# Performance work log

Hardware: AMD Instinct MI355X
Metric: run time of the kernel (lower is better)

Reference implementation:

```python
import jax, jax.numpy as jnp
import numpy as np

B, S = 64, 256
F, H, V = 512, 2048, 32000
PAD = 0
LN_EPS = 1e-5


def setup_inputs() -> dict:
    key = jax.random.key(0)
    ks = jax.random.split(key, 10)
    inputs = jax.random.randint(ks[0], (B, S), 0, V, dtype=jnp.int64)
    targets = jax.random.randint(ks[1], (B, S), 0, V, dtype=jnp.int64)
    # parameters (kaiming-ish / torch-default-ish scales)
    see = jax.random.normal(ks[2], (2 * F, F), jnp.float32) * (2.0 / (2 * F)) ** 0.5
    bias = jnp.zeros((F,), jnp.float32)
    W_in = jax.random.normal(ks[3], (H, F), jnp.float32) * (1.0 / F) ** 0.5
    b_in = jnp.zeros((H,), jnp.float32)
    W_out = jax.random.normal(ks[4], (F, H), jnp.float32) * (1.0 / H) ** 0.5
    b_out = jnp.zeros((F,), jnp.float32)
    ln_g = jnp.ones((F,), jnp.float32)
    ln_b = jnp.zeros((F,), jnp.float32)
    emb = jax.random.normal(ks[5], (V, F), jnp.float32)
    return {"inputs": inputs, "targets": targets, "see": see, "bias": bias,
            "W_in": W_in, "b_in": b_in, "W_out": W_out, "b_out": b_out,
            "ln_g": ln_g, "ln_b": ln_b, "emb": emb}


def _layernorm(x, g, b):
    mu = jnp.mean(x, axis=-1, keepdims=True)
    var = jnp.mean((x - mu) ** 2, axis=-1, keepdims=True)
    return (x - mu) * jax.lax.rsqrt(var + LN_EPS) * g + b


def reference(inputs, targets, see, bias, W_in, b_in, W_out, b_out, ln_g, ln_b, emb):
    emb_m = emb.at[PAD].set(0.0)  # padding_idx row is zero
    inv_sqrt_f = 1.0 / (F ** 0.5)

    def step(state, xy):
        idx, tgt = xy                      # [B], [B]
        vecs = emb_m[idx]                  # [B,F]
        gate = jax.nn.sigmoid(jnp.concatenate([vecs, state], axis=-1) @ see + bias)
        cont = state * gate + vecs * (1.0 - gate)
        h = jax.nn.relu(_layernorm(cont, ln_g, ln_b) @ W_in.T + b_in)
        out = h @ W_out.T + b_out          # [B,F]
        logits = (out @ emb_m.T) * inv_sqrt_f  # [B,V]
        logp = jax.nn.log_softmax(logits, axis=-1)
        nll = -jnp.take_along_axis(logp, tgt[:, None], axis=1)[:, 0]
        mask = (tgt != PAD).astype(logits.dtype)
        li = jnp.sum(nll * mask) / jnp.maximum(jnp.sum(mask), 1.0)
        return cont, li

    xs = (inputs.T, targets.T)  # [S,B]
    _, losses = jax.lax.scan(step, jnp.zeros((inputs.shape[0], F), emb.dtype), xs)
    return jnp.mean(losses)
```

## Files before the change

kernel.cpp:

```cpp
#include <hip/hip_runtime.h>
#include <hip/hip_fp8.h>

#define F_DIM 512
#define H_DIM 2048
#define V_DIM 32000
#define B_DIM 64
#define S_DIM 256
#define ROWS (S_DIM*B_DIM)
#define NT_LOG 250
#define SCALE 0.04419417382415922f
#define LSE_OFF 40.0f

typedef __attribute__((ext_vector_type(8))) short  short8;
typedef __attribute__((ext_vector_type(4))) float  floatx4;
typedef __attribute__((ext_vector_type(4))) int    intx4;
typedef __attribute__((ext_vector_type(8))) int    i32x8;
typedef __attribute__((ext_vector_type(4))) unsigned int uix4;

static __device__ inline unsigned short f2bf(float x){
  unsigned int u = __float_as_uint(x);
  u += 0x7fffu + ((u >> 16) & 1u);
  return (unsigned short)(u >> 16);
}
static __device__ inline float bf2f(unsigned short u){
  return __uint_as_float(((unsigned int)u) << 16);
}
static __device__ inline unsigned char f2fp8(float x){
  __hip_fp8_e4m3 q(x);
  return q.__x;
}
static __device__ inline int sw8(int row, int col){
  int g = (col >> 3) & 7;
  int chunk = ((g >> 1) ^ ((row >> 1) & 3));
  int lob = (g & 1) ^ ((row >> 3) & 1);
  return (col & ~63) | (chunk << 4) | (lob << 3) | (col & 7);
}
static __device__ inline int zvperm(int c){
  return (c & ~63) | ((c & 15) << 2) | ((c >> 4) & 3);
}
static __device__ inline float wsum(float v){
  #pragma unroll
  for(int m = 32; m > 0; m >>= 1) v += __shfl_xor(v, m);
  return v;
}
static __device__ inline void load_lds16(const void* g, void* l){
  __builtin_amdgcn_global_load_lds((const __attribute__((address_space(1))) void*)g,
                                   (__attribute__((address_space(3))) void*)l, 16, 0, 0);
}

__global__ __launch_bounds__(256) void cast_w(const float* __restrict__ src,
                                              unsigned short* __restrict__ dst, int n){
  int i = blockIdx.x*256 + threadIdx.x;
  int stride = gridDim.x*256;
  for(; i < n; i += stride) dst[i] = f2bf(src[i]);
}
__global__ __launch_bounds__(256) void cast_emb(const float* __restrict__ src,
    unsigned short* __restrict__ dst, unsigned char* __restrict__ d8){
  int i = blockIdx.x*256 + threadIdx.x;
  int stride = gridDim.x*256;
  for(; i < V_DIM*F_DIM; i += stride){
    float v = (i < F_DIM) ? 0.f : src[i];
    dst[i] = f2bf(v);
    int row = i >> 9, col = i & 511;
    d8[(long)row*512 + sw8(row, col)] = f2fp8(v);
  }
}

__global__ __launch_bounds__(256) void prep_see(const float* __restrict__ see,
    unsigned short* __restrict__ TT, unsigned char* __restrict__ B8){
  int n = blockIdx.x;
  for(int k = threadIdx.x; k < 512; k += 256){
    TT[n*512 + k] = f2bf(see[(long)k*512 + n]);
    B8[n*512 + k] = f2fp8(see[(long)(512+k)*512 + n]);
  }
}

__global__ __launch_bounds__(256) void gather_vecs(const float* __restrict__ emb,
    const int* __restrict__ inp, unsigned short* __restrict__ V){
  long row = (long)blockIdx.x*4 + (threadIdx.x >> 6);
  int l = threadIdx.x & 63;
  int t = (int)(row >> 6), b = (int)(row & 63);
  int idx = inp[b*S_DIM + t];
  short8 o;
  if (idx == 0){
    #pragma unroll
    for(int i=0;i<8;i++) o[i] = 0;
  } else {
    const float* e = emb + (long)idx*F_DIM + l*8;
    float4 a = *(const float4*)e;
    float4 bq = *(const float4*)(e + 4);
    o[0]=(short)f2bf(a.x); o[1]=(short)f2bf(a.y); o[2]=(short)f2bf(a.z); o[3]=(short)f2bf(a.w);
    o[4]=(short)f2bf(bq.x);o[5]=(short)f2bf(bq.y);o[6]=(short)f2bf(bq.z);o[7]=(short)f2bf(bq.w);
  }
  *(short8*)(V + row*F_DIM + l*8) = o;
}

__global__ __launch_bounds__(512, 1) void recurrence_batch(
    const unsigned int* __restrict__ ZV,
    const unsigned char* __restrict__ W8,
    unsigned short* __restrict__ CONTB)
{
  __shared__ unsigned char stt[2][16][560];

  const int tid = threadIdx.x;
  const int w  = tid >> 6;
  const int l  = tid & 63;
  const int rl = l & 15, rq = l >> 4;
  const int wg = blockIdx.x;
  const int colb = w*64;

  i32x8 Bfr[4][4];
  #pragma unroll
  for(int kt=0;kt<4;kt++)
    #pragma unroll
    for(int tl=0;tl<4;tl++)
      Bfr[kt][tl] = *(const i32x8*)(W8 + (long)(colb + tl*16 + rl)*512 + kt*128 + rq*32);

  float s_old[16];
  #pragma unroll
  for(int i=0;i<16;i++) s_old[i] = 0.f;

  const unsigned int* zbase = ZV + (long)(wg*16 + rq*4)*512 + colb + rl*4;
  unsigned short* cbase = CONTB + ((long)wg*16 + rq*4)*512 + colb + rl;

  uix4 zv[4];
  #pragma unroll
  for(int r=0;r<4;r++) zv[r] = *(const uix4*)(zbase + (long)r*512);

  for(int t = 0; t < S_DIM; t++){
    asm volatile("s_waitcnt lgkmcnt(0)" ::: "memory");
    __builtin_amdgcn_s_barrier();
    asm volatile("" ::: "memory");

    floatx4 acc[4];
    #pragma unroll
    for(int tl=0;tl<4;tl++) acc[tl] = (floatx4)0.f;

    i32x8 afr[4];
    if (t > 0){
      const unsigned char* sb = &stt[(t-1)&1][0][0] + rl*560 + rq*32;
      #pragma unroll
      for(int kt=0;kt<4;kt++){
        intx4 a0 = *(const intx4*)(sb + kt*128);
        intx4 a1 = *(const intx4*)(sb + kt*128 + 16);
        afr[kt] = __builtin_shufflevector(a0, a1, 0,1,2,3,4,5,6,7);
      }
    }

    unsigned short* cw = cbase + (long)t*64*512;
    unsigned char* swb = &stt[t&1][0][0] + rq*4*560 + colb + rl;

    #pragma unroll
    for(int tl=0;tl<4;tl++){
      if (t > 0){
        #pragma unroll
        for(int kt=0;kt<4;kt++)
          acc[tl] = __builtin_amdgcn_mfma_scale_f32_16x16x128_f8f6f4(
                        afr[kt], Bfr[kt][tl], acc[tl],
                        0, 0,
                        0, 0x7f7f7f7f,
                        0, 0x7f7f7f7f);
      }
      float sv[4];
      #pragma unroll
      for(int r=0;r<4;r++){
        unsigned int p = zv[r][tl];
        float z = __uint_as_float(p << 16) + acc[tl][r];
        float v = __uint_as_float(p & 0xffff0000u);
        float e = __expf(-z);
        float g = __builtin_amdgcn_rcpf(1.f + e);
        float s = fmaf(s_old[tl*4+r] - v, g, v);
        s_old[tl*4+r] = s;
        sv[r] = s;
      }
      #pragma unroll
      for(int pr=0; pr<2; pr++){
        unsigned int bfp, f8p;
        asm("v_cvt_pk_bf16_f32 %0, %1, %2" : "=v"(bfp) : "v"(sv[pr*2]), "v"(sv[pr*2+1]));
        asm("v_cvt_pk_fp8_f32 %0, %1, %2"  : "=v"(f8p) : "v"(sv[pr*2]), "v"(sv[pr*2+1]));
        cw[(long)(pr*2)*512   + tl*16] = (unsigned short)(bfp & 0xffffu);
        cw[(long)(pr*2+1)*512 + tl*16] = (unsigned short)(bfp >> 16);
        swb[(pr*2)*560   + tl*16] = (unsigned char)(f8p & 0xffu);
        swb[(pr*2+1)*560 + tl*16] = (unsigned char)((f8p >> 8) & 0xffu);
      }
    }

    if (t+1 < S_DIM){
      const unsigned int* zp = zbase + (long)(t+1)*64*512;
      #pragma unroll
      for(int r=0;r<4;r++) zv[r] = *(const uix4*)(zp + (long)r*512);
    }
  }
}

__global__ __launch_bounds__(256) void ln_kernel(const unsigned short* __restrict__ contb,
    const float* __restrict__ lg, const float* __restrict__ lb,
    unsigned short* __restrict__ xln)
{
  const int wid = threadIdx.x >> 6, l = threadIdx.x & 63;
  const long row = (long)blockIdx.x*4 + wid;
  short8 xv = *(const short8*)(contb + row*F_DIM + l*8);
  float v[8];
  #pragma unroll
  for(int i=0;i<8;i++) v[i] = bf2f((unsigned short)xv[i]);
  float s = 0.f;
  #pragma unroll
  for(int i=0;i<8;i++) s += v[i];
  s = wsum(s);
  float mu = s * (1.f/512.f);
  float q = 0.f;
  #pragma unroll
  for(int i=0;i<8;i++){ float d = v[i]-mu; q += d*d; }
  q = wsum(q);
  float rs = rsqrtf(q*(1.f/512.f) + 1e-5f);
  short8 o;
  #pragma unroll
  for(int i=0;i<8;i++)
    o[i] = (short)f2bf((v[i]-mu)*rs*lg[l*8+i] + lb[l*8+i]);
  *(short8*)(xln + row*F_DIM + l*8) = o;
}

template<int MODE>
__global__ __launch_bounds__(256) void gemm_bt(
    const unsigned short* __restrict__ A,
    const unsigned short* __restrict__ Bm,
    const float* __restrict__ bias,
    unsigned short* __restrict__ C,
    unsigned char* __restrict__ C8,
    const unsigned short* __restrict__ Vsrc,
    unsigned int* __restrict__ ZVout,
    int M, int N, int K, int tiles_m, int tiles_n)
{
  __shared__ short As[128*64];
  __shared__ short Bs[128*64];

  const int bid = blockIdx.x;
  const int mt = bid % tiles_m;
  const int nt = bid / tiles_m;
  const long m0 = (long)mt * 128;
  const long n0 = (long)nt * 128;
  const int tid = threadIdx.x;
  const int l = tid & 63;
  const int wid = tid >> 6;
  const int wr = wid >> 1, wc = wid & 1;
  const int rl = l & 15, rq = l >> 4;

  const short* Ag = (const short*)A + m0 * K;
  const short* Bg = (const short*)Bm + n0 * K;
  const int grow = tid >> 3;
  const int kp = tid & 7;
  const int ksw = (kp ^ (grow & 7)) * 8;

  floatx4 acc[4][4];
  #pragma unroll
  for(int i=0;i<4;i++)
    #pragma unroll
    for(int j=0;j<4;j++) acc[i][j] = (floatx4)0.f;

  for(int k0 = 0; k0 < K; k0 += 64){
    __syncthreads();
    #pragma unroll
    for(int ro = 0; ro < 128; ro += 32){
      load_lds16(Ag + (long)(ro + grow)*K + k0 + ksw, (void*)(As + (ro+grow)*64 + kp*8));
      load_lds16(Bg + (long)(ro + grow)*K + k0 + ksw, (void*)(Bs + (ro+grow)*64 + kp*8));
    }
    __syncthreads();
    #pragma unroll
    for(int kb = 0; kb < 64; kb += 32){
      const int cb = kb >> 3;
      const int cl = ((cb + rq) ^ (rl & 7)) * 8;
      short8 af[4], bfr[4];
      #pragma unroll
      for(int i=0;i<4;i++) af[i]  = *(const short8*)(As + (wr*64 + i*16 + rl)*64 + cl);
      #pragma unroll
      for(int j=0;j<4;j++) bfr[j] = *(const short8*)(Bs + (wc*64 + j*16 + rl)*64 + cl);
      #pragma unroll
      for(int i=0;i<4;i++)
        #pragma unroll
        for(int j=0;j<4;j++)
          acc[i][j] = __builtin_amdgcn_mfma_f32_16x16x32_bf16(af[i], bfr[j], acc[i][j], 0, 0, 0);
    }
  }

  const long mb = m0 + wr*64;
  const long nb = n0 + wc*64;
  #pragma unroll
  for(int j=0;j<4;j++){
    float bj = bias[nb + j*16 + rl];
    #pragma unroll
    for(int i=0;i<4;i++){
      #pragma unroll
      for(int r=0;r<4;r++){
        float v = acc[i][j][r] + bj;
        if (MODE == 0) v = fmaxf(v, 0.f);
        int rowI = (int)(mb + i*16 + rq*4 + r);
        int colI = (int)(nb + j*16 + rl);
        long idx = (long)rowI*N + colI;
        if (MODE == 5){
          ZVout[(long)rowI*N + zvperm(colI)] =
              ((unsigned)Vsrc[idx] << 16) | (unsigned)f2bf(v);
        } else {
          C[idx] = f2bf(v);
          if (MODE == 4) C8[(long)rowI*512 + sw8(rowI, colI)] = f2fp8(v);
        }
      }
    }
  }
}

__global__ __launch_bounds__(256) void gemm_f8_logits(
    const unsigned char* __restrict__ A8,
    const unsigned char* __restrict__ B8,
    float* __restrict__ part,
    int M, int N, int K, int tiles_m, int tiles_n)
{
  __shared__ unsigned char As8[2][128*64];
  __shared__ unsigned char Bs8[2][128*64];
  __shared__ float sm2[2][64][2];

  const int bid = blockIdx.x;
  const int mt = bid % tiles_m;
  const int nt = bid / tiles_m;
  const long m0 = (long)mt * 128;
  const long n0 = (long)nt * 128;
  const int tid = threadIdx.x;
  const int l = tid & 63;
  const int wid = tid >> 6;
  const int wr = wid >> 1, wc = wid & 1;
  const int rl = l & 15, rq = l >> 4;

  const unsigned char* Ag = A8 + m0 * K;
  const unsigned char* Bg = B8 + n0 * K;
  const int grow = tid >> 2;
  const int kp = tid & 3;

  floatx4 acc[4][4];
  #pragma unroll
  for(int i=0;i<4;i++)
    #pragma unroll
    for(int j=0;j<4;j++) acc[i][j] = (floatx4)0.f;

  const int rsw = (rl >> 1) & 3;
  const int rhi = (rl >> 3) & 1;

  const int nkt = K >> 6;

  #define STAGE_F8(bb, kk) do {                                               \
    const long kof = (long)(kk)*64 + kp*16;                                   \
    load_lds16(Ag + (long)grow*K       + kof, (void*)(&As8[bb][grow*64       + kp*16])); \
    load_lds16(Ag + (long)(64+grow)*K  + kof, (void*)(&As8[bb][(64+grow)*64  + kp*16])); \
    load_lds16(Bg + (long)grow*K       + kof, (void*)(&Bs8[bb][grow*64       + kp*16])); \
    load_lds16(Bg + (long)(64+grow)*K  + kof, (void*)(&Bs8[bb][(64+grow)*64  + kp*16])); \
  } while(0)

  STAGE_F8(0, 0);
  STAGE_F8(1, 1);

  for(int t = 0; t < nkt; t++){
    if (t < nkt-1) asm volatile("s_waitcnt vmcnt(4)" ::: "memory");
    else           asm volatile("s_waitcnt vmcnt(0)" ::: "memory");
    __builtin_amdgcn_s_barrier();
    __builtin_amdgcn_sched_barrier(0);

    const unsigned char* Abuf = &As8[t & 1][0];
    const unsigned char* Bbuf = &Bs8[t & 1][0];
    long af[2][4], bfr[2][4];
    #pragma unroll
    for(int kb = 0; kb < 2; kb++){
      const int g = (kb << 2) + rq;
      const int cl = ((((g >> 1) ^ rsw)) << 4) | ((((g & 1) ^ rhi)) << 3);
      #pragma unroll
      for(int i=0;i<4;i++) af[kb][i]  = *(const long*)(Abuf + (wr*64 + i*16 + rl)*64 + cl);
      #pragma unroll
      for(int j=0;j<4;j++) bfr[kb][j] = *(const long*)(Bbuf + (wc*64 + j*16 + rl)*64 + cl);
    }
    asm volatile("s_waitcnt lgkmcnt(0)" ::: "memory");
    __builtin_amdgcn_sched_barrier(0);
    __builtin_amdgcn_s_barrier();
    __builtin_amdgcn_sched_barrier(0);

    if (t+2 < nkt) STAGE_F8(t & 1, t+2);

    __builtin_amdgcn_s_setprio(1);
    #pragma unroll
    for(int kb = 0; kb < 2; kb++)
      #pragma unroll
      for(int i=0;i<4;i++)
        #pragma unroll
        for(int j=0;j<4;j++)
          acc[i][j] = __builtin_amdgcn_mfma_f32_16x16x32_fp8_fp8(af[kb][i], bfr[kb][j], acc[i][j], 0, 0, 0);
    __builtin_amdgcn_s_setprio(0);
  }
  #undef STAGE_F8

  #pragma unroll
  for(int i=0;i<4;i++){
    #pragma unroll
    for(int r=0;r<4;r++){
      float sv = 0.f;
      #pragma unroll
      for(int j=0;j<4;j++) sv += __expf(acc[i][j][r]*SCALE - LSE_OFF);
      #pragma unroll
      for(int d=1; d<16; d<<=1) sv += __shfl_xor(sv, d);
      if (rl == 0) sm2[wr][i*16 + rq*4 + r][wc] = sv;
    }
  }
  __syncthreads();
  if (tid < 128){
    int wr2 = tid >> 6, rowl = tid & 63;
    part[(m0 + wr2*64 + rowl)*tiles_n + nt] = sm2[wr2][rowl][0] + sm2[wr2][rowl][1];
  }
}

__global__ __launch_bounds__(256) void tlogit_kernel(const unsigned short* __restrict__ outb,
    const unsigned short* __restrict__ embb, const int* __restrict__ tgt,
    float* __restrict__ TL)
{
  long gw = (long)blockIdx.x*4 + (threadIdx.x >> 6);
  int l = threadIdx.x & 63;
  int t = (int)(gw >> 6), b = (int)(gw & 63);
  int tg = tgt[b*S_DIM + t];
  const unsigned short* o = outb + gw*F_DIM;
  const unsigned short* e = embb + (long)tg*F_DIM;
  short8 ov = *(const short8*)(o + l*8);
  short8 ev = *(const short8*)(e + l*8);
  float s = 0.f;
  #pragma unroll
  for(int i=0;i<8;i++) s += bf2f((unsigned short)ov[i]) * bf2f((unsigned short)ev[i]);
  s = wsum(s);
  if (l == 0) TL[gw] = s * SCALE;
}

__global__ __launch_bounds__(256) void lse_kernel(const float* __restrict__ part,
    const float* __restrict__ TL, float* __restrict__ nll)
{
  long row = (long)blockIdx.x*4 + (threadIdx.x >> 6);
  int l = threadIdx.x & 63;
  float S = 0.f;
  for(int c = l; c < NT_LOG; c += 64)
    S += part[row*NT_LOG + c];
  S = wsum(S);
  if (l == 0) nll[row] = (LSE_OFF + logf(S)) - TL[row];
}

__global__ __launch_bounds__(256) void loss_kernel(const float* __restrict__ nll,
    const int* __restrict__ tgt, float* __restrict__ out)
{
  int t = threadIdx.x;
  float s = 0.f; int cnt = 0;
  for(int b = 0; b < B_DIM; b++){
    int v = tgt[b*S_DIM + t];
    if (v != 0){ s += nll[(long)t*B_DIM + b]; cnt++; }
  }
  float li = s / fmaxf((float)cnt, 1.f);
  li = wsum(li);
  __shared__ float red[4];
  if ((t & 63) == 0) red[t >> 6] = li;
  __syncthreads();
  if (t == 0) out[0] = (red[0]+red[1]+red[2]+red[3]) * (1.f/256.f);
}

extern "C" void kernel_launch(void* const* d_in, const int* in_sizes, int n_in,
                              void* d_out, int out_size, void* d_ws, size_t ws_size,
                              hipStream_t stream)
{
  const int*   inp   = (const int*)d_in[0];
  const int*   tgt   = (const int*)d_in[1];
  const float* see   = (const float*)d_in[2];
  const float* bias  = (const float*)d_in[3];
  const float* W_in  = (const float*)d_in[4];
  const float* b_in  = (const float*)d_in[5];
  const float* W_out = (const float*)d_in[6];
  const float* b_out = (const float*)d_in[7];
  const float* ln_g  = (const float*)d_in[8];
  const float* ln_b  = (const float*)d_in[9];
  const float* emb   = (const float*)d_in[10];

  char* p = (char*)d_ws;
  unsigned short* CONTB= (unsigned short*)p; p += (size_t)ROWS*F_DIM*2;
  unsigned short* Hb   = (unsigned short*)p; p += (size_t)ROWS*H_DIM*2;
  unsigned short* OUTb = (unsigned short*)p; p += (size_t)ROWS*F_DIM*2;
  unsigned short* EMBb = (unsigned short*)p; p += (size_t)V_DIM*F_DIM*2;
  unsigned char* EMB8  = (unsigned char*)p;  p += (size_t)V_DIM*F_DIM;
  unsigned short* WINb = (unsigned short*)p; p += (size_t)H_DIM*F_DIM*2;
  unsigned short* WOUTb= (unsigned short*)p; p += (size_t)F_DIM*H_DIM*2;
  float* TL            = (float*)p;          p += (size_t)ROWS*4;
  float* NLL           = (float*)p;          p += (size_t)ROWS*4;
  unsigned short* VECSb= (unsigned short*)p; p += (size_t)ROWS*F_DIM*2;
  unsigned int* ZV     = (unsigned int*)p;   p += (size_t)ROWS*F_DIM*4;
  unsigned short* SEETT= (unsigned short*)p; p += (size_t)F_DIM*F_DIM*2;
  unsigned char* SEEB8 = (unsigned char*)p;  p += (size_t)F_DIM*F_DIM;
  unsigned short* XLN  = (unsigned short*)ZV;
  unsigned char* OUT8  = (unsigned char*)VECSb;
  float* PART          = (float*)Hb;

  cast_emb<<<4096, 256, 0, stream>>>(emb, EMBb, EMB8);
  cast_w<<<2048, 256, 0, stream>>>(W_in,  WINb,  H_DIM*F_DIM);
  cast_w<<<2048, 256, 0, stream>>>(W_out, WOUTb, F_DIM*H_DIM);
  prep_see<<<512, 256, 0, stream>>>(see, SEETT, SEEB8);
  gather_vecs<<<ROWS/4, 256, 0, stream>>>(emb, inp, VECSb);

  gemm_bt<5><<<128*4, 256, 0, stream>>>(VECSb, SEETT, bias, nullptr, nullptr,
                                        VECSb, ZV, ROWS, F_DIM, F_DIM, 128, 4);

  recurrence_batch<<<4, 512, 0, stream>>>(ZV, SEEB8, CONTB);

  ln_kernel<<<ROWS/4, 256, 0, stream>>>(CONTB, ln_g, ln_b, XLN);
  gemm_bt<0><<<128*16, 256, 0, stream>>>(XLN,  WINb,  b_in,  Hb,   nullptr,
                                         nullptr, nullptr, ROWS, H_DIM, F_DIM, 128, 16);
  gemm_bt<4><<<128*4,  256, 0, stream>>>(Hb,   WOUTb, b_out, OUTb, OUT8,
                                         nullptr, nullptr, ROWS, F_DIM, H_DIM, 128, 4);
  tlogit_kernel<<<ROWS/4, 256, 0, stream>>>(OUTb, EMBb, tgt, TL);
  gemm_f8_logits<<<128*NT_LOG, 256, 0, stream>>>(OUT8, EMB8, PART, ROWS, V_DIM, F_DIM, 128, NT_LOG);
  lse_kernel<<<ROWS/4, 256, 0, stream>>>(PART, TL, NLL);
  loss_kernel<<<1, 256, 0, stream>>>(NLL, tgt, (float*)d_out);
}
```

Baseline: 1.151 ms.

## Use gfx950 16x16x128 scaled FP8 MFMA in logits GEMM with K=128 stages

Switches the FP8 logits GEMM from the 16x16x32 fp8 MFMA to the gfx950 mfma_scale 16x16x128 f8f6f4 instruction with unit scales. Each k-tile now covers 128 and is staged as two 64-wide swizzled segments, and each lane gathers 32 bytes per operand. This quarters the MFMA instruction count and halves barrier rounds per K. In exchange it doubles LDS usage per buffer and makes the per-lane fragment gather more complex, which risks bank conflicts or wrong k ordering if the lane-to-k mapping does not match the instruction layout.

```diff
diff --git a/kernel.cpp b/kernel.cpp
--- a/kernel.cpp
+++ b/kernel.cpp
@@ -46,6 +46,12 @@
 static __device__ inline void load_lds16(const void* g, void* l){
   __builtin_amdgcn_global_load_lds((const __attribute__((address_space(1))) void*)g,
                                    (__attribute__((address_space(3))) void*)l, 16, 0, 0);
+}
+static __device__ inline i32x8 asm8(long a, long b, long c, long d){
+  i32x8 r;
+  r[0]=(int)a; r[1]=(int)(a>>32); r[2]=(int)b; r[3]=(int)(b>>32);
+  r[4]=(int)c; r[5]=(int)(c>>32); r[6]=(int)d; r[7]=(int)(d>>32);
+  return r;
 }
 
 __global__ __launch_bounds__(256) void cast_w(const float* __restrict__ src,
@@ -314,8 +320,8 @@
     float* __restrict__ part,
     int M, int N, int K, int tiles_m, int tiles_n)
 {
-  __shared__ unsigned char As8[2][128*64];
-  __shared__ unsigned char Bs8[2][128*64];
+  __shared__ unsigned char As8[2][2][128*64];
+  __shared__ unsigned char Bs8[2][2][128*64];
   __shared__ float sm2[2][64][2];
 
   const int bid = blockIdx.x;
@@ -342,37 +348,51 @@
 
   const int rsw = (rl >> 1) & 3;
   const int rhi = (rl >> 3) & 1;
-
-  const int nkt = K >> 6;
+  const int seg = rq >> 1;
+  int cl[4];
+  #pragma unroll
+  for(int j=0;j<4;j++){
+    int g = ((rq & 1) << 2) + j;
+    cl[j] = ((((g >> 1) ^ rsw)) << 4) | (((g & 1) ^ rhi) << 3);
+  }
+
+  const int nkt = K >> 7;
 
   #define STAGE_F8(bb, kk) do {                                               \
-    const long kof = (long)(kk)*64 + kp*16;                                   \
-    load_lds16(Ag + (long)grow*K       + kof, (void*)(&As8[bb][grow*64       + kp*16])); \
-    load_lds16(Ag + (long)(64+grow)*K  + kof, (void*)(&As8[bb][(64+grow)*64  + kp*16])); \
-    load_lds16(Bg + (long)grow*K       + kof, (void*)(&Bs8[bb][grow*64       + kp*16])); \
-    load_lds16(Bg + (long)(64+grow)*K  + kof, (void*)(&Bs8[bb][(64+grow)*64  + kp*16])); \
+    const long kof = (long)(kk)*128 + kp*16;                                  \
+    load_lds16(Ag + (long)grow*K      + kof,      (void*)(&As8[bb][0][grow*64      + kp*16])); \
+    load_lds16(Ag + (long)(64+grow)*K + kof,      (void*)(&As8[bb][0][(64+grow)*64 + kp*16])); \
+    load_lds16(Ag + (long)grow*K      + kof + 64, (void*)(&As8[bb][1][grow*64      + kp*16])); \
+    load_lds16(Ag + (long)(64+grow)*K + kof + 64, (void*)(&As8[bb][1][(64+grow)*64 + kp*16])); \
+    load_lds16(Bg + (long)grow*K      + kof,      (void*)(&Bs8[bb][0][grow*64      + kp*16])); \
+    load_lds16(Bg + (long)(64+grow)*K + kof,      (void*)(&Bs8[bb][0][(64+grow)*64 + kp*16])); \
+    load_lds16(Bg + (long)grow*K      + kof + 64, (void*)(&Bs8[bb][1][grow*64      + kp*16])); \
+    load_lds16(Bg + (long)(64+grow)*K + kof + 64, (void*)(&Bs8[bb][1][(64+grow)*64 + kp*16])); \
   } while(0)
 
   STAGE_F8(0, 0);
   STAGE_F8(1, 1);
 
   for(int t = 0; t < nkt; t++){
-    if (t < nkt-1) asm volatile("s_waitcnt vmcnt(4)" ::: "memory");
+    if (t < nkt-1) asm volatile("s_waitcnt vmcnt(8)" ::: "memory");
     else           asm volatile("s_waitcnt vmcnt(0)" ::: "memory");
     __builtin_amdgcn_s_barrier();
     __builtin_amdgcn_sched_barrier(0);
 
-    const unsigned char* Abuf = &As8[t & 1][0];
-    const unsigned char* Bbuf = &Bs8[t & 1][0];
-    long af[2][4], bfr[2][4];
-    #pragma unroll
-    for(int kb = 0; kb < 2; kb++){
-      const int g = (kb << 2) + rq;
-      const int cl = ((((g >> 1) ^ rsw)) << 4) | ((((g & 1) ^ rhi)) << 3);
-      #pragma unroll
-      for(int i=0;i<4;i++) af[kb][i]  = *(const long*)(Abuf + (wr*64 + i*16 + rl)*64 + cl);
-      #pragma unroll
-      for(int j=0;j<4;j++) bfr[kb][j] = *(const long*)(Bbuf + (wc*64 + j*16 + rl)*64 + cl);
+    const unsigned char* Aseg = &As8[t & 1][seg][0];
+    const unsigned char* Bseg = &Bs8[t & 1][seg][0];
+    i32x8 af[4], bfv[4];
+    #pragma unroll
+    for(int i=0;i<4;i++){
+      const unsigned char* rb = Aseg + (wr*64 + i*16 + rl)*64;
+      af[i] = asm8(*(const long*)(rb + cl[0]), *(const long*)(rb + cl[1]),
+                   *(const long*)(rb + cl[2]), *(const long*)(rb + cl[3]));
+    }
+    #pragma unroll
+    for(int j=0;j<4;j++){
+      const unsigned char* rb = Bseg + (wc*64 + j*16 + rl)*64;
+      bfv[j] = asm8(*(const long*)(rb + cl[0]), *(const long*)(rb + cl[1]),
+                    *(const long*)(rb + cl[2]), *(const long*)(rb + cl[3]));
     }
     asm volatile("s_waitcnt lgkmcnt(0)" ::: "memory");
     __builtin_amdgcn_sched_barrier(0);
@@ -383,12 +403,12 @@
 
     __builtin_amdgcn_s_setprio(1);
     #pragma unroll
-    for(int kb = 0; kb < 2; kb++)
-      #pragma unroll
-      for(int i=0;i<4;i++)
-        #pragma unroll
-        for(int j=0;j<4;j++)
-          acc[i][j] = __builtin_amdgcn_mfma_f32_16x16x32_fp8_fp8(af[kb][i], bfr[kb][j], acc[i][j], 0, 0, 0);
+    for(int i=0;i<4;i++)
+      #pragma unroll
+      for(int j=0;j<4;j++)
+        acc[i][j] = __builtin_amdgcn_mfma_scale_f32_16x16x128_f8f6f4(
+                        af[i], bfv[j], acc[i][j],
+                        0, 0, 0, 0x7f7f7f7f, 0, 0x7f7f7f7f);
     __builtin_amdgcn_s_setprio(0);
   }
   #undef STAGE_F8
```

After: 1.263 ms. +9.8%, slower.
